# Performance work log

Hardware: AMD Instinct MI355X
Metric: run time of the kernel (lower is better)

Reference implementation:

```python
import jax, jax.numpy as jnp
import numpy as np

B, N, C = 4, 4096, 1024
H = 16
HD = C // H            # 64
HID = 4 * C            # 4096
EPS_LN = 1e-5
EPS_ATTN = 1e-6


def layernorm(x, w, b):
    mu = jnp.mean(x, axis=-1, keepdims=True)
    var = jnp.mean((x - mu) ** 2, axis=-1, keepdims=True)
    return (x - mu) * jax.lax.rsqrt(var + EPS_LN) * w + b


def setup_inputs() -> dict:
    key = jax.random.key(0)
    ks = jax.random.split(key, 12)
    s_in = 1.0 / np.sqrt(C)
    s_hid = 1.0 / np.sqrt(HID)
    return {
        "x": jax.random.normal(ks[0], (B, N, C), jnp.float32),
        "ln1_w": jnp.ones((C,), jnp.float32),
        "ln1_b": jnp.zeros((C,), jnp.float32),
        "ln2_w": jnp.ones((C,), jnp.float32),
        "ln2_b": jnp.zeros((C,), jnp.float32),
        "qkv_w": jax.random.uniform(ks[1], (3 * C, C), jnp.float32, -s_in, s_in),
        "qkv_b": jax.random.uniform(ks[2], (3 * C,), jnp.float32, -s_in, s_in),
        "out_w": jax.random.uniform(ks[3], (C, C), jnp.float32, -s_in, s_in),
        "out_b": jax.random.uniform(ks[4], (C,), jnp.float32, -s_in, s_in),
        "fc1_w": jax.random.uniform(ks[5], (HID, C), jnp.float32, -s_in, s_in),
        "fc1_b": jax.random.uniform(ks[6], (HID,), jnp.float32, -s_in, s_in),
        "fc2_w": jax.random.uniform(ks[7], (C, HID), jnp.float32, -s_hid, s_hid),
        "fc2_b": jax.random.uniform(ks[8], (C,), jnp.float32, -s_hid, s_hid),
    }


def linear_attention(x, qkv_w, qkv_b, out_w, out_b):
    b, n, c = x.shape
    qkv = x @ qkv_w.T + qkv_b                       # [B,N,3C]
    # rearrange 'b n (h d) -> b h n d' with d = 3*HD, then chunk into q,k,v
    qkv = qkv.reshape(b, n, H, 3 * HD).transpose(0, 2, 1, 3)  # [B,H,N,3*HD]
    q, k, v = jnp.split(qkv, 3, axis=-1)            # each [B,H,N,HD]
    q = jax.nn.silu(q)
    k = jax.nn.silu(k)
    state = jnp.einsum('bhnd,bhne->bhde', k, v)     # k^T @ v, [B,H,HD,HD]
    k_sum = jnp.sum(k, axis=2)                      # [B,H,HD]
    num = jnp.einsum('bhnd,bhde->bhne', q, state)   # [B,H,N,HD]
    den = jnp.einsum('bhnd,bhd->bhn', q, k_sum)[..., None]
    out = num / (den + EPS_ATTN)
    out = out.transpose(0, 2, 1, 3).reshape(b, n, c)
    return out @ out_w.T + out_b


def reference(x, ln1_w, ln1_b, ln2_w, ln2_b, qkv_w, qkv_b, out_w, out_b,
              fc1_w, fc1_b, fc2_w, fc2_b):
    x = x + linear_attention(layernorm(x, ln1_w, ln1_b), qkv_w, qkv_b, out_w, out_b)
    h = layernorm(x, ln2_w, ln2_b)
    h = jax.nn.gelu(h @ fc1_w.T + fc1_b, approximate=False)
    return x + (h @ fc2_w.T + fc2_b)
```

## Files before the change

### kernel.cpp

```cpp
#include <hip/hip_runtime.h>
#include <hip/hip_bf16.h>
#include <math.h>

typedef __bf16 bf16x8 __attribute__((ext_vector_type(8)));
typedef _Float16 f16x8 __attribute__((ext_vector_type(8)));
typedef float  f32x4  __attribute__((ext_vector_type(4)));

#define GLB_AS(p) ((const __attribute__((address_space(1))) void*)(p))
#define LDS_AS(p) ((__attribute__((address_space(3))) void*)(p))

__device__ __forceinline__ double shfl_xor_dbl(double v, int m) {
    union { double d; int i[2]; } u;
    u.d = v;
    u.i[0] = __shfl_xor(u.i[0], m);
    u.i[1] = __shfl_xor(u.i[1], m);
    return u.d;
}

__global__ __launch_bounds__(256) void cvt_kernel(const float* __restrict__ in,
                                                  __hip_bfloat16* __restrict__ o) {
    const int i = blockIdx.x * 256 + threadIdx.x;
    const float4 v = ((const float4*)in)[i];
    __hip_bfloat16* p = o + (size_t)i * 4;
    p[0] = __float2bfloat16(v.x);
    p[1] = __float2bfloat16(v.y);
    p[2] = __float2bfloat16(v.z);
    p[3] = __float2bfloat16(v.w);
}

template <int OFS, bool HAS_LO>
__global__ __launch_bounds__(256) void cvt_split_kernel(const float* __restrict__ w,
                                                        _Float16* __restrict__ hi,
                                                        _Float16* __restrict__ lo) {
    const int j = blockIdx.x;
    const int src = (j >> 6) * 192 + OFS + (j & 63);
    const float4 v = ((const float4*)(w + (size_t)src * 1024))[threadIdx.x];
    _Float16 h0 = (_Float16)v.x, h1 = (_Float16)v.y, h2 = (_Float16)v.z, h3 = (_Float16)v.w;
    _Float16* hp = hi + (size_t)j * 1024 + threadIdx.x * 4;
    hp[0] = h0; hp[1] = h1; hp[2] = h2; hp[3] = h3;
    if (HAS_LO) {
        _Float16* lp = lo + (size_t)j * 1024 + threadIdx.x * 4;
        lp[0] = (_Float16)((v.x - (float)h0) * 1024.f);
        lp[1] = (_Float16)((v.y - (float)h1) * 1024.f);
        lp[2] = (_Float16)((v.z - (float)h2) * 1024.f);
        lp[3] = (_Float16)((v.w - (float)h3) * 1024.f);
    }
}

__global__ __launch_bounds__(256) void ln_split_kernel(const float* __restrict__ x,
                                                       const float* __restrict__ w,
                                                       const float* __restrict__ b,
                                                       _Float16* __restrict__ yh,
                                                       _Float16* __restrict__ yl) {
    const int row = blockIdx.x;
    const int t = threadIdx.x;
    const float4 v = ((const float4*)(x + (size_t)row * 1024))[t];
    float s1 = v.x + v.y + v.z + v.w;
    float s2 = v.x * v.x + v.y * v.y + v.z * v.z + v.w * v.w;
#pragma unroll
    for (int off = 32; off; off >>= 1) {
        s1 += __shfl_xor(s1, off);
        s2 += __shfl_xor(s2, off);
    }
    __shared__ float red[8];
    const int wid = t >> 6, lane = t & 63;
    if (lane == 0) { red[wid] = s1; red[4 + wid] = s2; }
    __syncthreads();
    s1 = red[0] + red[1] + red[2] + red[3];
    s2 = red[4] + red[5] + red[6] + red[7];
    const float mu = s1 * (1.f / 1024.f);
    const float var = s2 * (1.f / 1024.f) - mu * mu;
    const float rs = rsqrtf(var + 1e-5f);
    const float4 wv = ((const float4*)w)[t];
    const float4 bv = ((const float4*)b)[t];
    float y[4] = {(v.x - mu) * rs * wv.x + bv.x, (v.y - mu) * rs * wv.y + bv.y,
                  (v.z - mu) * rs * wv.z + bv.z, (v.w - mu) * rs * wv.w + bv.w};
    _Float16* hp = yh + (size_t)row * 1024 + t * 4;
    _Float16* lp = yl + (size_t)row * 1024 + t * 4;
#pragma unroll
    for (int j = 0; j < 4; ++j) {
        _Float16 h = (_Float16)y[j];
        hp[j] = h;
        lp[j] = (_Float16)((y[j] - (float)h) * 1024.f);
    }
}

__global__ __launch_bounds__(256) void ln_kernel(const float* __restrict__ x,
                                                 const float* __restrict__ w,
                                                 const float* __restrict__ b,
                                                 __hip_bfloat16* __restrict__ y) {
    const int row = blockIdx.x;
    const int t = threadIdx.x;
    const float4 v = ((const float4*)(x + (size_t)row * 1024))[t];
    float s1 = v.x + v.y + v.z + v.w;
    float s2 = v.x * v.x + v.y * v.y + v.z * v.z + v.w * v.w;
#pragma unroll
    for (int off = 32; off; off >>= 1) {
        s1 += __shfl_xor(s1, off);
        s2 += __shfl_xor(s2, off);
    }
    __shared__ float red[8];
    const int wid = t >> 6, lane = t & 63;
    if (lane == 0) { red[wid] = s1; red[4 + wid] = s2; }
    __syncthreads();
    s1 = red[0] + red[1] + red[2] + red[3];
    s2 = red[4] + red[5] + red[6] + red[7];
    const float mu = s1 * (1.f / 1024.f);
    const float var = s2 * (1.f / 1024.f) - mu * mu;
    const float rs = rsqrtf(var + 1e-5f);
    const float4 wv = ((const float4*)w)[t];
    const float4 bv = ((const float4*)b)[t];
    __hip_bfloat16* yp = y + (size_t)row * 1024 + t * 4;
    yp[0] = __float2bfloat16((v.x - mu) * rs * wv.x + bv.x);
    yp[1] = __float2bfloat16((v.y - mu) * rs * wv.y + bv.y);
    yp[2] = __float2bfloat16((v.z - mu) * rs * wv.z + bv.z);
    yp[3] = __float2bfloat16((v.w - mu) * rs * wv.w + bv.w);
}

template <int EPI>
__global__ __launch_bounds__(256) void gemm_f16(const _Float16* __restrict__ Ah,
                                                const _Float16* __restrict__ Al,
                                                const _Float16* __restrict__ Bh,
                                                const _Float16* __restrict__ Bl,
                                                const float* __restrict__ qkvb,
                                                _Float16* __restrict__ outp,
                                                const double* __restrict__ ksum_in,
                                                float* __restrict__ kpart,
                                                double* __restrict__ den_out) {
    const int K = 1024;
    constexpr int KSPLIT = (EPI == 0) ? 512 : 1024;
    __shared__ __align__(16) _Float16 AsH[128 * 32];
    __shared__ __align__(16) _Float16 BsH[128 * 32];
    __shared__ __align__(16) _Float16 AsL[128 * 32];
    __shared__ __align__(16) _Float16 BsL[128 * 32];
    __shared__ float kl[8][128];
    const int tid = threadIdx.x;
    const int wid = tid >> 6;
    const int lane = tid & 63;
    const int bm = blockIdx.x, bn = blockIdx.y;
    const int wr = (wid >> 1) * 64;
    const int wc = (wid & 1) * 64;
    const int l15 = lane & 15;
    const int lhi = lane >> 4;

    f32x4 acc0a[4][4] = {};
    f32x4 acc0b[4][4] = {};
    f32x4 acc1[4][4] = {};

    const int row0 = tid >> 2, colb0 = (tid & 3) * 16;
    const size_t rowstride = (size_t)K * 2;
    const char* AhB = (const char*)(Ah + (size_t)(bm * 128) * K);
    const char* BhB = (const char*)(Bh + (size_t)(bn * 128) * K);
    const char* AlB = (const char*)(Al + (size_t)(bm * 128) * K);
    const char* BlB = (const char*)(Bl + (size_t)(bn * 128) * K);

    auto kstep = [&](int k0, f32x4 (&accH)[4][4]) {
        const size_t koff = (size_t)k0 * 2;
        const size_t o0 = (size_t)row0 * rowstride + koff + colb0;
        const size_t o1 = o0 + 64 * rowstride;
        __builtin_amdgcn_global_load_lds(GLB_AS(AhB + o0), LDS_AS((char*)AsH + wid * 1024), 16, 0, 0);
        __builtin_amdgcn_global_load_lds(GLB_AS(AhB + o1), LDS_AS((char*)AsH + 4096 + wid * 1024), 16, 0, 0);
        __builtin_amdgcn_global_load_lds(GLB_AS(BhB + o0), LDS_AS((char*)BsH + wid * 1024), 16, 0, 0);
        __builtin_amdgcn_global_load_lds(GLB_AS(BhB + o1), LDS_AS((char*)BsH + 4096 + wid * 1024), 16, 0, 0);
        if (EPI < 2) {
            __builtin_amdgcn_global_load_lds(GLB_AS(AlB + o0), LDS_AS((char*)AsL + wid * 1024), 16, 0, 0);
            __builtin_amdgcn_global_load_lds(GLB_AS(AlB + o1), LDS_AS((char*)AsL + 4096 + wid * 1024), 16, 0, 0);
            __builtin_amdgcn_global_load_lds(GLB_AS(BlB + o0), LDS_AS((char*)BsL + wid * 1024), 16, 0, 0);
            __builtin_amdgcn_global_load_lds(GLB_AS(BlB + o1), LDS_AS((char*)BsL + 4096 + wid * 1024), 16, 0, 0);
        }
        __syncthreads();

        f16x8 ah[4], bh[4], al[4], bl[4];
#pragma unroll
        for (int m = 0; m < 4; ++m) {
            ah[m] = *(const f16x8*)(AsH + (wr + m * 16 + l15) * 32 + lhi * 8);
            if (EPI < 2) al[m] = *(const f16x8*)(AsL + (wr + m * 16 + l15) * 32 + lhi * 8);
        }
#pragma unroll
        for (int n = 0; n < 4; ++n) {
            bh[n] = *(const f16x8*)(BsH + (wc + n * 16 + l15) * 32 + lhi * 8);
            if (EPI < 2) bl[n] = *(const f16x8*)(BsL + (wc + n * 16 + l15) * 32 + lhi * 8);
        }
#pragma unroll
        for (int m = 0; m < 4; ++m)
#pragma unroll
            for (int n = 0; n < 4; ++n) {
                accH[m][n] = __builtin_amdgcn_mfma_f32_16x16x32_f16(ah[m], bh[n], accH[m][n], 0, 0, 0);
                if (EPI < 2) {
                    acc1[m][n] = __builtin_amdgcn_mfma_f32_16x16x32_f16(ah[m], bl[n], acc1[m][n], 0, 0, 0);
                    acc1[m][n] = __builtin_amdgcn_mfma_f32_16x16x32_f16(al[m], bh[n], acc1[m][n], 0, 0, 0);
                }
            }
        __syncthreads();
    };

    for (int k0 = 0; k0 < KSPLIT; k0 += 32) kstep(k0, acc0a);
    for (int k0 = KSPLIT; k0 < K; k0 += 32) kstep(k0, acc0b);

    const int rbase = bm * 128 + wr + lhi * 4;
    const int j0 = bn * 128 + wc + l15;
    const int hh = (bn * 128 + wc) >> 6;
    const int bofs = (EPI == 0) ? 0 : (EPI == 1) ? 64 : 128;
    const int bb = (bm * 128) >> 12;
    const int kbase = bb * 1024 + hh * 64;

    double ks[4];
    if (EPI == 0) {
#pragma unroll
        for (int n = 0; n < 4; ++n) ks[n] = ksum_in[kbase + n * 16 + l15];
    }
    double kcol[4] = {};

#pragma unroll
    for (int m = 0; m < 4; ++m) {
#pragma unroll
        for (int i = 0; i < 4; ++i) {
            const int gr = rbase + m * 16 + i;
            double denv = 0.0;
#pragma unroll
            for (int n = 0; n < 4; ++n) {
                double qd = (double)acc0a[m][n][i] + (double)acc0b[m][n][i];
                if (EPI < 2) qd += (double)acc1[m][n][i] * (1.0 / 1024.0);
                qd += (double)qkvb[hh * 192 + bofs + n * 16 + l15];
                if (EPI < 2) {
                    const double sd = qd / (1.0 + exp(-qd));
                    outp[(size_t)gr * 1024 + j0 + n * 16] = (_Float16)(float)sd;
                    if (EPI == 0) denv += sd * ks[n];
                    if (EPI == 1) kcol[n] += sd;
                } else {
                    outp[(size_t)gr * 1024 + j0 + n * 16] = (_Float16)(float)qd;
                }
            }
            if (EPI == 0) {
                denv += shfl_xor_dbl(denv, 1);
                denv += shfl_xor_dbl(denv, 2);
                denv += shfl_xor_dbl(denv, 4);
                denv += shfl_xor_dbl(denv, 8);
                if (l15 == 0) den_out[(size_t)gr * 16 + hh] = denv;
            }
        }
    }
    if (EPI == 1) {
        const int part = (wr >> 6) * 4 + lhi;
#pragma unroll
        for (int n = 0; n < 4; ++n) kl[part][wc + n * 16 + l15] = (float)kcol[n];
        __syncthreads();
        if (tid < 128) {
            double s = 0.0;
#pragma unroll
            for (int p = 0; p < 8; ++p) s += (double)kl[p][tid];
            kpart[(size_t)bm * 1024 + bn * 128 + tid] = (float)s;
        }
    }
}

__global__ __launch_bounds__(256) void ksum_reduce_kernel(const float* __restrict__ kpart,
                                                          double* __restrict__ ksum) {
    const int idx = blockIdx.x * 256 + threadIdx.x;
    const int b = idx >> 10, col = idx & 1023;
    double acc = 0.0;
    for (int j = 0; j < 32; ++j) acc += (double)kpart[(size_t)(b * 32 + j) * 1024 + col];
    ksum[idx] = acc;
}

template <int EPI>
__global__ __launch_bounds__(256) void gemm_bt(const __hip_bfloat16* __restrict__ A,
                                               const __hip_bfloat16* __restrict__ Bt,
                                               const float* __restrict__ bias,
                                               const float* __restrict__ resid,
                                               void* __restrict__ outp,
                                               int M, int N, int K) {
    __shared__ __align__(16) __hip_bfloat16 As[128 * 32];
    __shared__ __align__(16) __hip_bfloat16 Bs[128 * 32];
    const int tid = threadIdx.x;
    const int wid = tid >> 6;
    const int lane = tid & 63;
    const int bm = blockIdx.x, bn = blockIdx.y;
    const int wr = (wid >> 1) * 64;
    const int wc = (wid & 1) * 64;
    const int l15 = lane & 15;
    const int lhi = lane >> 4;

    f32x4 acc[4][4] = {};

    const int row0 = tid >> 2, colb0 = (tid & 3) * 16;
    const char* Abase = (const char*)(A + (size_t)(bm * 128) * K);
    const char* Bbase = (const char*)(Bt + (size_t)(bn * 128) * K);
    const size_t rowstride = (size_t)K * 2;

    for (int k0 = 0; k0 < K; k0 += 32) {
        const size_t koff = (size_t)k0 * 2;
        const size_t o0 = (size_t)row0 * rowstride + koff + colb0;
        const size_t o1 = o0 + 64 * rowstride;
        __builtin_amdgcn_global_load_lds(GLB_AS(Abase + o0), LDS_AS((char*)As + wid * 1024), 16, 0, 0);
        __builtin_amdgcn_global_load_lds(GLB_AS(Abase + o1), LDS_AS((char*)As + 4096 + wid * 1024), 16, 0, 0);
        __builtin_amdgcn_global_load_lds(GLB_AS(Bbase + o0), LDS_AS((char*)Bs + wid * 1024), 16, 0, 0);
        __builtin_amdgcn_global_load_lds(GLB_AS(Bbase + o1), LDS_AS((char*)Bs + 4096 + wid * 1024), 16, 0, 0);
        __syncthreads();

        bf16x8 af[4], bf[4];
#pragma unroll
        for (int m = 0; m < 4; ++m)
            af[m] = *(const bf16x8*)(As + (wr + m * 16 + l15) * 32 + lhi * 8);
#pragma unroll
        for (int n = 0; n < 4; ++n)
            bf[n] = *(const bf16x8*)(Bs + (wc + n * 16 + l15) * 32 + lhi * 8);
#pragma unroll
        for (int m = 0; m < 4; ++m)
#pragma unroll
            for (int n = 0; n < 4; ++n)
                acc[m][n] = __builtin_amdgcn_mfma_f32_16x16x32_bf16(af[m], bf[n], acc[m][n], 0, 0, 0);
        __syncthreads();
    }

    const int rbase = bm * 128 + wr + lhi * 4;
    const int cbase = bn * 128 + wc + l15;
#pragma unroll
    for (int n = 0; n < 4; ++n) {
        const int gc = cbase + n * 16;
        const float bv = bias[gc];
#pragma unroll
        for (int m = 0; m < 4; ++m) {
#pragma unroll
            for (int i = 0; i < 4; ++i) {
                const int gr = rbase + m * 16 + i;
                const size_t o = (size_t)gr * N + gc;
                float v = acc[m][n][i] + bv;
                if (EPI == 1) {
                    ((float*)outp)[o] = v + resid[o];
                } else {
                    v = 0.5f * v * (1.f + erff(v * 0.70710678118f));
                    ((__hip_bfloat16*)outp)[o] = __float2bfloat16(v);
                }
            }
        }
    }
}

__global__ __launch_bounds__(256) void attn_state_kernel(const _Float16* __restrict__ Kf,
                                                         const _Float16* __restrict__ Vf,
                                                         float* __restrict__ s8) {
    const int bh = blockIdx.x;
    const int b = bh >> 4, h = bh & 15;
    const int n0 = blockIdx.y * 512;
    __shared__ float klds[64][64];
    __shared__ float vlds[64][64];
    const int t = threadIdx.x;
    const int r = t >> 2, cc = (t & 3) * 16;
    const int d = t >> 2, e0 = (t & 3) * 16;
    float s[16] = {};

    for (int c = 0; c < 512; c += 64) {
        const size_t m = (size_t)b * 4096 + n0 + c + r;
        const _Float16* kb = Kf + m * 1024 + h * 64;
        const _Float16* vb = Vf + m * 1024 + h * 64;
        const f16x8 k0 = *(const f16x8*)(kb + cc);
        const f16x8 k1 = *(const f16x8*)(kb + cc + 8);
        const f16x8 v0 = *(const f16x8*)(vb + cc);
        const f16x8 v1 = *(const f16x8*)(vb + cc + 8);
        __syncthreads();
#pragma unroll
        for (int j = 0; j < 8; ++j) {
            klds[r][cc + j]     = (float)k0[j];
            klds[r][cc + 8 + j] = (float)k1[j];
            vlds[r][cc + j]     = (float)v0[j];
            vlds[r][cc + 8 + j] = (float)v1[j];
        }
        __syncthreads();
#pragma unroll 8
        for (int n = 0; n < 64; ++n) {
            const float kk = klds[n][d];
            const float4* vp = (const float4*)&vlds[n][e0];
            const float4 a0 = vp[0], a1 = vp[1], a2 = vp[2], a3 = vp[3];
            s[0]  += kk * a0.x; s[1]  += kk * a0.y; s[2]  += kk * a0.z; s[3]  += kk * a0.w;
            s[4]  += kk * a1.x; s[5]  += kk * a1.y; s[6]  += kk * a1.z; s[7]  += kk * a1.w;
            s[8]  += kk * a2.x; s[9]  += kk * a2.y; s[10] += kk * a2.z; s[11] += kk * a2.w;
            s[12] += kk * a3.x; s[13] += kk * a3.y; s[14] += kk * a3.z; s[15] += kk * a3.w;
        }
    }
    float* sp = s8 + (((size_t)blockIdx.y * 64 + bh) * 64 + d) * 64 + e0;
#pragma unroll
    for (int j = 0; j < 16; ++j) sp[j] = s[j];
}

__global__ __launch_bounds__(256) void state_reduce_kernel(const float* __restrict__ s8,
                                                           float* __restrict__ state) {
    const int idx = blockIdx.x * 256 + threadIdx.x;
    float a = 0.f;
#pragma unroll
    for (int j = 0; j < 8; ++j) a += s8[(size_t)j * 262144 + idx];
    state[idx] = a;
}

__global__ __launch_bounds__(256) void attn_out_kernel(const _Float16* __restrict__ Qf,
                                                       const float* __restrict__ state,
                                                       const double* __restrict__ den,
                                                       __hip_bfloat16* __restrict__ aout) {
    const int bh = blockIdx.x;
    const int b = bh >> 4, h = bh & 15;
    const int n0 = blockIdx.y * 64;
    __shared__ float slds[64][64];
    __shared__ float qlds[64][65];
    const int t = threadIdx.x;
    {
        const float4* sp = (const float4*)(state + (size_t)bh * 4096);
        float4* dp = (float4*)&slds[0][0];
#pragma unroll
        for (int i = 0; i < 4; ++i) dp[i * 256 + t] = sp[i * 256 + t];
    }
    {
        const int r = t >> 2, cc = (t & 3) * 16;
        const size_t m = (size_t)b * 4096 + n0 + r;
        const _Float16* qb = Qf + m * 1024 + h * 64;
        const f16x8 q0 = *(const f16x8*)(qb + cc);
        const f16x8 q1 = *(const f16x8*)(qb + cc + 8);
#pragma unroll
        for (int j = 0; j < 8; ++j) {
            qlds[r][cc + j]     = (float)q0[j];
            qlds[r][cc + 8 + j] = (float)q1[j];
        }
    }
    __syncthreads();
    const int r = t >> 2, e0 = (t & 3) * 16;
    const size_t mrow = (size_t)b * 4096 + n0 + r;
    float o[16] = {};
#pragma unroll 8
    for (int dd = 0; dd < 64; ++dd) {
        const float qv = qlds[r][dd];
        const float4* sp4 = (const float4*)&slds[dd][e0];
        const float4 a0 = sp4[0], a1 = sp4[1], a2 = sp4[2], a3 = sp4[3];
        o[0]  += qv * a0.x; o[1]  += qv * a0.y; o[2]  += qv * a0.z; o[3]  += qv * a0.w;
        o[4]  += qv * a1.x; o[5]  += qv * a1.y; o[6]  += qv * a1.z; o[7]  += qv * a1.w;
        o[8]  += qv * a2.x; o[9]  += qv * a2.y; o[10] += qv * a2.z; o[11] += qv * a2.w;
        o[12] += qv * a3.x; o[13] += qv * a3.y; o[14] += qv * a3.z; o[15] += qv * a3.w;
    }
    const float inv = (float)(1.0 / (den[mrow * 16 + h] + 1e-6));
    __hip_bfloat16* op = aout + mrow * 1024 + h * 64 + e0;
#pragma unroll
    for (int j = 0; j < 16; ++j) op[j] = __float2bfloat16(o[j] * inv);
}

extern "C" void kernel_launch(void* const* d_in, const int* in_sizes, int n_in,
                              void* d_out, int out_size, void* d_ws, size_t ws_size,
                              hipStream_t stream) {
    const float* x     = (const float*)d_in[0];
    const float* ln1_w = (const float*)d_in[1];
    const float* ln1_b = (const float*)d_in[2];
    const float* ln2_w = (const float*)d_in[3];
    const float* ln2_b = (const float*)d_in[4];
    const float* qkv_w = (const float*)d_in[5];
    const float* qkv_b = (const float*)d_in[6];
    const float* out_w = (const float*)d_in[7];
    const float* out_b = (const float*)d_in[8];
    const float* fc1_w = (const float*)d_in[9];
    const float* fc1_b = (const float*)d_in[10];
    const float* fc2_w = (const float*)d_in[11];
    const float* fc2_b = (const float*)d_in[12];
    float* out = (float*)d_out;

    char* ws = (char*)d_ws;
    _Float16* Wqh = (_Float16*)(ws + 0);
    _Float16* Wql = (_Float16*)(ws + 2097152);
    _Float16* Wkh = (_Float16*)(ws + 4194304);
    _Float16* Wkl = (_Float16*)(ws + 6291456);
    _Float16* Wvh = (_Float16*)(ws + 8388608);
    __hip_bfloat16* Wo = (__hip_bfloat16*)(ws + 10485760);
    __hip_bfloat16* W1 = (__hip_bfloat16*)(ws + 12582912);
    __hip_bfloat16* W2 = (__hip_bfloat16*)(ws + 20971520);
    _Float16* XH = (_Float16*)(ws + 29360128);
    _Float16* XL = (_Float16*)(ws + 62914560);
    _Float16* QF = (_Float16*)(ws + 96468992);
    _Float16* KF = (_Float16*)(ws + 130023424);
    _Float16* VF = (_Float16*)(ws + 163577856);
    double* DEN  = (double*)(ws + 197132288);
    float* KPART = (float*)(ws + 199229440);
    double* KSUM = (double*)(ws + 199753728);
    float* STATE = (float*)(ws + 199786496);
    float* STATE8 = (float*)XH;
    __hip_bfloat16* AO   = (__hip_bfloat16*)XL;
    __hip_bfloat16* Hbuf = (__hip_bfloat16*)XL;
    __hip_bfloat16* XN2  = (__hip_bfloat16*)XH;

    cvt_split_kernel<0, true><<<1024, 256, 0, stream>>>(qkv_w, Wqh, Wql);
    cvt_split_kernel<64, true><<<1024, 256, 0, stream>>>(qkv_w, Wkh, Wkl);
    cvt_split_kernel<128, false><<<1024, 256, 0, stream>>>(qkv_w, Wvh, nullptr);
    cvt_kernel<<<1024, 256, 0, stream>>>(out_w, Wo);
    cvt_kernel<<<4096, 256, 0, stream>>>(fc1_w, W1);
    cvt_kernel<<<4096, 256, 0, stream>>>(fc2_w, W2);

    ln_split_kernel<<<16384, 256, 0, stream>>>(x, ln1_w, ln1_b, XH, XL);

    gemm_f16<1><<<dim3(128, 8), 256, 0, stream>>>(XH, XL, Wkh, Wkl, qkv_b, KF, nullptr, KPART, nullptr);
    ksum_reduce_kernel<<<16, 256, 0, stream>>>(KPART, KSUM);
    gemm_f16<0><<<dim3(128, 8), 256, 0, stream>>>(XH, XL, Wqh, Wql, qkv_b, QF, KSUM, nullptr, DEN);
    gemm_f16<2><<<dim3(128, 8), 256, 0, stream>>>(XH, nullptr, Wvh, nullptr, qkv_b, VF, nullptr, nullptr, nullptr);

    attn_state_kernel<<<dim3(64, 8), 256, 0, stream>>>(KF, VF, STATE8);
    state_reduce_kernel<<<1024, 256, 0, stream>>>(STATE8, STATE);
    attn_out_kernel<<<dim3(64, 64), 256, 0, stream>>>(QF, STATE, DEN, AO);

    gemm_bt<1><<<dim3(128, 8), 256, 0, stream>>>(AO, Wo, out_b, x, out, 16384, 1024, 1024);
    ln_kernel<<<16384, 256, 0, stream>>>(out, ln2_w, ln2_b, XN2);
    gemm_bt<2><<<dim3(128, 32), 256, 0, stream>>>(XN2, W1, fc1_b, nullptr, Hbuf, 16384, 4096, 1024);
    gemm_bt<1><<<dim3(128, 8), 256, 0, stream>>>(Hbuf, W2, fc2_b, out, out, 16384, 1024, 4096);
}
```

Baseline: 1.454 ms.

## Double-buffer LDS in GEMMs with async prefetch and XCD-aware block remap

All GEMM kernels (the split-f16 QKV ones and the bf16 output/MLP ones) now keep two LDS buffers. The next K-tile is issued with global_load_lds while the current tile is computed, and explicit vmcnt waits plus barriers replace the per-step syncthreads pair. This is meant to hide global-load latency behind MFMA work. The launch grid becomes 1D, and block indices are remapped so consecutive tiles spread across the 8 XCDs for better L2 locality. K and N become template constants, and LDS use doubles (64KB for the split kernels), which may reduce occupancy.

```diff
diff --git a/kernel.cpp b/kernel.cpp
--- a/kernel.cpp
+++ b/kernel.cpp
@@ -8,6 +8,10 @@
 
 #define GLB_AS(p) ((const __attribute__((address_space(1))) void*)(p))
 #define LDS_AS(p) ((__attribute__((address_space(3))) void*)(p))
+
+__device__ __forceinline__ void gll16(const void* g, void* l) {
+    __builtin_amdgcn_global_load_lds(GLB_AS(g), LDS_AS(l), 16, 0, 0);
+}
 
 __device__ __forceinline__ double shfl_xor_dbl(double v, int m) {
     union { double d; int i[2]; } u;
@@ -127,17 +131,16 @@
                                                 const double* __restrict__ ksum_in,
                                                 float* __restrict__ kpart,
                                                 double* __restrict__ den_out) {
-    const int K = 1024;
-    constexpr int KSPLIT = (EPI == 0) ? 512 : 1024;
-    __shared__ __align__(16) _Float16 AsH[128 * 32];
-    __shared__ __align__(16) _Float16 BsH[128 * 32];
-    __shared__ __align__(16) _Float16 AsL[128 * 32];
-    __shared__ __align__(16) _Float16 BsL[128 * 32];
+    constexpr int K = 1024;
+    constexpr int NT = 32;
+    __shared__ __align__(16) char SM[(EPI < 2) ? 65536 : 32768];
     __shared__ float kl[8][128];
     const int tid = threadIdx.x;
     const int wid = tid >> 6;
     const int lane = tid & 63;
-    const int bm = blockIdx.x, bn = blockIdx.y;
+    const int nwg = gridDim.x;
+    const int wg = (blockIdx.x & 7) * (nwg >> 3) + (blockIdx.x >> 3);
+    const int bm = wg >> 3, bn = wg & 7;
     const int wr = (wid >> 1) * 64;
     const int wc = (wid & 1) * 64;
     const int l15 = lane & 15;
@@ -148,38 +151,45 @@
     f32x4 acc1[4][4] = {};
 
     const int row0 = tid >> 2, colb0 = (tid & 3) * 16;
-    const size_t rowstride = (size_t)K * 2;
+    constexpr size_t rowstride = (size_t)K * 2;
     const char* AhB = (const char*)(Ah + (size_t)(bm * 128) * K);
     const char* BhB = (const char*)(Bh + (size_t)(bn * 128) * K);
     const char* AlB = (const char*)(Al + (size_t)(bm * 128) * K);
     const char* BlB = (const char*)(Bl + (size_t)(bn * 128) * K);
 
-    auto kstep = [&](int k0, f32x4 (&accH)[4][4]) {
-        const size_t koff = (size_t)k0 * 2;
-        const size_t o0 = (size_t)row0 * rowstride + koff + colb0;
+    auto STAGE = [&](int db, int s) {
+        const size_t o0 = (size_t)row0 * rowstride + (size_t)s * 64 + colb0;
         const size_t o1 = o0 + 64 * rowstride;
-        __builtin_amdgcn_global_load_lds(GLB_AS(AhB + o0), LDS_AS((char*)AsH + wid * 1024), 16, 0, 0);
-        __builtin_amdgcn_global_load_lds(GLB_AS(AhB + o1), LDS_AS((char*)AsH + 4096 + wid * 1024), 16, 0, 0);
-        __builtin_amdgcn_global_load_lds(GLB_AS(BhB + o0), LDS_AS((char*)BsH + wid * 1024), 16, 0, 0);
-        __builtin_amdgcn_global_load_lds(GLB_AS(BhB + o1), LDS_AS((char*)BsH + 4096 + wid * 1024), 16, 0, 0);
+        char* AH = SM + db * 8192;
+        char* BH = SM + 16384 + db * 8192;
+        gll16(AhB + o0, AH + wid * 1024);
+        gll16(AhB + o1, AH + 4096 + wid * 1024);
+        gll16(BhB + o0, BH + wid * 1024);
+        gll16(BhB + o1, BH + 4096 + wid * 1024);
         if (EPI < 2) {
-            __builtin_amdgcn_global_load_lds(GLB_AS(AlB + o0), LDS_AS((char*)AsL + wid * 1024), 16, 0, 0);
-            __builtin_amdgcn_global_load_lds(GLB_AS(AlB + o1), LDS_AS((char*)AsL + 4096 + wid * 1024), 16, 0, 0);
-            __builtin_amdgcn_global_load_lds(GLB_AS(BlB + o0), LDS_AS((char*)BsL + wid * 1024), 16, 0, 0);
-            __builtin_amdgcn_global_load_lds(GLB_AS(BlB + o1), LDS_AS((char*)BsL + 4096 + wid * 1024), 16, 0, 0);
-        }
-        __syncthreads();
-
+            char* AL = SM + 32768 + db * 8192;
+            char* BL = SM + 49152 + db * 8192;
+            gll16(AlB + o0, AL + wid * 1024);
+            gll16(AlB + o1, AL + 4096 + wid * 1024);
+            gll16(BlB + o0, BL + wid * 1024);
+            gll16(BlB + o1, BL + 4096 + wid * 1024);
+        }
+    };
+    auto COMPUTE = [&](int db, f32x4 (&accH)[4][4]) {
+        const _Float16* AH = (const _Float16*)(SM + db * 8192);
+        const _Float16* BH = (const _Float16*)(SM + 16384 + db * 8192);
+        const _Float16* AL = (const _Float16*)(SM + 32768 + db * 8192);
+        const _Float16* BL = (const _Float16*)(SM + 49152 + db * 8192);
         f16x8 ah[4], bh[4], al[4], bl[4];
 #pragma unroll
         for (int m = 0; m < 4; ++m) {
-            ah[m] = *(const f16x8*)(AsH + (wr + m * 16 + l15) * 32 + lhi * 8);
-            if (EPI < 2) al[m] = *(const f16x8*)(AsL + (wr + m * 16 + l15) * 32 + lhi * 8);
+            ah[m] = *(const f16x8*)(AH + (wr + m * 16 + l15) * 32 + lhi * 8);
+            if (EPI < 2) al[m] = *(const f16x8*)(AL + (wr + m * 16 + l15) * 32 + lhi * 8);
         }
 #pragma unroll
         for (int n = 0; n < 4; ++n) {
-            bh[n] = *(const f16x8*)(BsH + (wc + n * 16 + l15) * 32 + lhi * 8);
-            if (EPI < 2) bl[n] = *(const f16x8*)(BsL + (wc + n * 16 + l15) * 32 + lhi * 8);
+            bh[n] = *(const f16x8*)(BH + (wc + n * 16 + l15) * 32 + lhi * 8);
+            if (EPI < 2) bl[n] = *(const f16x8*)(BL + (wc + n * 16 + l15) * 32 + lhi * 8);
         }
 #pragma unroll
         for (int m = 0; m < 4; ++m)
@@ -191,11 +201,26 @@
                     acc1[m][n] = __builtin_amdgcn_mfma_f32_16x16x32_f16(al[m], bh[n], acc1[m][n], 0, 0, 0);
                 }
             }
-        __syncthreads();
     };
 
-    for (int k0 = 0; k0 < KSPLIT; k0 += 32) kstep(k0, acc0a);
-    for (int k0 = KSPLIT; k0 < K; k0 += 32) kstep(k0, acc0b);
+    STAGE(0, 0);
+    for (int s = 0; s < NT - 1; ++s) {
+        const int cur = s & 1;
+        STAGE(cur ^ 1, s + 1);
+        if (EPI < 2) asm volatile("s_waitcnt vmcnt(8)" ::: "memory");
+        else         asm volatile("s_waitcnt vmcnt(4)" ::: "memory");
+        __builtin_amdgcn_s_barrier();
+        __builtin_amdgcn_sched_barrier(0);
+        if (EPI == 0 && s >= 16) COMPUTE(cur, acc0b);
+        else                     COMPUTE(cur, acc0a);
+        __builtin_amdgcn_sched_barrier(0);
+        __builtin_amdgcn_s_barrier();
+    }
+    asm volatile("s_waitcnt vmcnt(0)" ::: "memory");
+    __builtin_amdgcn_s_barrier();
+    __builtin_amdgcn_sched_barrier(0);
+    if (EPI == 0) COMPUTE((NT - 1) & 1, acc0b);
+    else          COMPUTE((NT - 1) & 1, acc0a);
 
     const int rbase = bm * 128 + wr + lhi * 4;
     const int j0 = bn * 128 + wc + l15;
@@ -263,19 +288,21 @@
     ksum[idx] = acc;
 }
 
-template <int EPI>
+template <int EPI, int N, int K>
 __global__ __launch_bounds__(256) void gemm_bt(const __hip_bfloat16* __restrict__ A,
                                                const __hip_bfloat16* __restrict__ Bt,
                                                const float* __restrict__ bias,
                                                const float* __restrict__ resid,
-                                               void* __restrict__ outp,
-                                               int M, int N, int K) {
-    __shared__ __align__(16) __hip_bfloat16 As[128 * 32];
-    __shared__ __align__(16) __hip_bfloat16 Bs[128 * 32];
+                                               void* __restrict__ outp) {
+    constexpr int NT = K / 32;
+    constexpr int NBN = N / 128;
+    __shared__ __align__(16) char SM[2 * 16384];
     const int tid = threadIdx.x;
     const int wid = tid >> 6;
     const int lane = tid & 63;
-    const int bm = blockIdx.x, bn = blockIdx.y;
+    const int nwg = gridDim.x;
+    const int wg = (blockIdx.x & 7) * (nwg >> 3) + (blockIdx.x >> 3);
+    const int bm = wg / NBN, bn = wg % NBN;
     const int wr = (wid >> 1) * 64;
     const int wc = (wid & 1) * 64;
     const int l15 = lane & 15;
@@ -286,32 +313,50 @@
     const int row0 = tid >> 2, colb0 = (tid & 3) * 16;
     const char* Abase = (const char*)(A + (size_t)(bm * 128) * K);
     const char* Bbase = (const char*)(Bt + (size_t)(bn * 128) * K);
-    const size_t rowstride = (size_t)K * 2;
-
-    for (int k0 = 0; k0 < K; k0 += 32) {
-        const size_t koff = (size_t)k0 * 2;
-        const size_t o0 = (size_t)row0 * rowstride + koff + colb0;
+    constexpr size_t rowstride = (size_t)K * 2;
+
+    auto STAGE = [&](int db, int s) {
+        const size_t o0 = (size_t)row0 * rowstride + (size_t)s * 64 + colb0;
         const size_t o1 = o0 + 64 * rowstride;
-        __builtin_amdgcn_global_load_lds(GLB_AS(Abase + o0), LDS_AS((char*)As + wid * 1024), 16, 0, 0);
-        __builtin_amdgcn_global_load_lds(GLB_AS(Abase + o1), LDS_AS((char*)As + 4096 + wid * 1024), 16, 0, 0);
-        __builtin_amdgcn_global_load_lds(GLB_AS(Bbase + o0), LDS_AS((char*)Bs + wid * 1024), 16, 0, 0);
-        __builtin_amdgcn_global_load_lds(GLB_AS(Bbase + o1), LDS_AS((char*)Bs + 4096 + wid * 1024), 16, 0, 0);
-        __syncthreads();
-
-        bf16x8 af[4], bf[4];
+        char* As = SM + db * 16384;
+        char* Bs = As + 8192;
+        gll16(Abase + o0, As + wid * 1024);
+        gll16(Abase + o1, As + 4096 + wid * 1024);
+        gll16(Bbase + o0, Bs + wid * 1024);
+        gll16(Bbase + o1, Bs + 4096 + wid * 1024);
+    };
+    auto COMPUTE = [&](int db) {
+        const __hip_bfloat16* As = (const __hip_bfloat16*)(SM + db * 16384);
+        const __hip_bfloat16* Bs = As + 4096;
+        bf16x8 af[4], bf4[4];
 #pragma unroll
         for (int m = 0; m < 4; ++m)
             af[m] = *(const bf16x8*)(As + (wr + m * 16 + l15) * 32 + lhi * 8);
 #pragma unroll
         for (int n = 0; n < 4; ++n)
-            bf[n] = *(const bf16x8*)(Bs + (wc + n * 16 + l15) * 32 + lhi * 8);
+            bf4[n] = *(const bf16x8*)(Bs + (wc + n * 16 + l15) * 32 + lhi * 8);
 #pragma unroll
         for (int m = 0; m < 4; ++m)
 #pragma unroll
             for (int n = 0; n < 4; ++n)
-                acc[m][n] = __builtin_amdgcn_mfma_f32_16x16x32_bf16(af[m], bf[n], acc[m][n], 0, 0, 0);
-        __syncthreads();
-    }
+                acc[m][n] = __builtin_amdgcn_mfma_f32_16x16x32_bf16(af[m], bf4[n], acc[m][n], 0, 0, 0);
+    };
+
+    STAGE(0, 0);
+    for (int s = 0; s < NT - 1; ++s) {
+        const int cur = s & 1;
+        STAGE(cur ^ 1, s + 1);
+        asm volatile("s_waitcnt vmcnt(4)" ::: "memory");
+        __builtin_amdgcn_s_barrier();
+        __builtin_amdgcn_sched_barrier(0);
+        COMPUTE(cur);
+        __builtin_amdgcn_sched_barrier(0);
+        __builtin_amdgcn_s_barrier();
+    }
+    asm volatile("s_waitcnt vmcnt(0)" ::: "memory");
+    __builtin_amdgcn_s_barrier();
+    __builtin_amdgcn_sched_barrier(0);
+    COMPUTE((NT - 1) & 1);
 
     const int rbase = bm * 128 + wr + lhi * 4;
     const int cbase = bn * 128 + wc + l15;
@@ -490,17 +535,17 @@
 
     ln_split_kernel<<<16384, 256, 0, stream>>>(x, ln1_w, ln1_b, XH, XL);
 
-    gemm_f16<1><<<dim3(128, 8), 256, 0, stream>>>(XH, XL, Wkh, Wkl, qkv_b, KF, nullptr, KPART, nullptr);
+    gemm_f16<1><<<1024, 256, 0, stream>>>(XH, XL, Wkh, Wkl, qkv_b, KF, nullptr, KPART, nullptr);
     ksum_reduce_kernel<<<16, 256, 0, stream>>>(KPART, KSUM);
-    gemm_f16<0><<<dim3(128, 8), 256, 0, stream>>>(XH, XL, Wqh, Wql, qkv_b, QF, KSUM, nullptr, DEN);
-    gemm_f16<2><<<dim3(128, 8), 256, 0, stream>>>(XH, nullptr, Wvh, nullptr, qkv_b, VF, nullptr, nullptr, nullptr);
+    gemm_f16<0><<<1024, 256, 0, stream>>>(XH, XL, Wqh, Wql, qkv_b, QF, KSUM, nullptr, DEN);
+    gemm_f16<2><<<1024, 256, 0, stream>>>(XH, nullptr, Wvh, nullptr, qkv_b, VF, nullptr, nullptr, nullptr);
 
     attn_state_kernel<<<dim3(64, 8), 256, 0, stream>>>(KF, VF, STATE8);
     state_reduce_kernel<<<1024, 256, 0, stream>>>(STATE8, STATE);
     attn_out_kernel<<<dim3(64, 64), 256, 0, stream>>>(QF, STATE, DEN, AO);
 
-    gemm_bt<1><<<dim3(128, 8), 256, 0, stream>>>(AO, Wo, out_b, x, out, 16384, 1024, 1024);
+    gemm_bt<1, 1024, 1024><<<1024, 256, 0, stream>>>(AO, Wo, out_b, x, out);
     ln_kernel<<<16384, 256, 0, stream>>>(out, ln2_w, ln2_b, XN2);
-    gemm_bt<2><<<dim3(128, 32), 256, 0, stream>>>(XN2, W1, fc1_b, nullptr, Hbuf, 16384, 4096, 1024);
-    gemm_bt<1><<<dim3(128, 8), 256, 0, stream>>>(Hbuf, W2, fc2_b, out, out, 16384, 1024, 4096);
-}
+    gemm_bt<2, 4096, 1024><<<4096, 256, 0, stream>>>(XN2, W1, fc1_b, nullptr, Hbuf);
+    gemm_bt<1, 1024, 4096><<<1024, 256, 0, stream>>>(Hbuf, W2, fc2_b, out, out);
+}
```

Result: faster. 1.277 ms (-12.2%).
